# Kernel optimization log

Hardware: AMD Instinct MI355X
Metric: run time of the kernel (lower is better)

## Reference

```python
import jax, jax.numpy as jnp
import numpy as np

B, L, D = 8, 4096, 2048
E, TOPK, RANK = 8, 2, 8
ALPHA = 1.0 / RANK
LN_EPS = 1e-5


def setup_inputs() -> dict:
    key = jax.random.key(0)
    ks = jax.random.split(key, 7)
    return {
        "x": jax.random.normal(ks[0], (B, L, D), dtype=jnp.float32),
        "gate_w": jax.random.normal(ks[1], (E, D), dtype=jnp.float32) * 0.02,
        "gate_b": jax.random.normal(ks[2], (E,), dtype=jnp.float32) * 0.02,
        "A": jax.random.normal(ks[3], (E, RANK, D), dtype=jnp.float32) * 0.02,
        "Bw": jax.random.normal(ks[4], (E, D, RANK), dtype=jnp.float32) * 0.02,
        "gamma": 1.0 + 0.1 * jax.random.normal(ks[5], (D,), dtype=jnp.float32),
        "beta": 0.1 * jax.random.normal(ks[6], (D,), dtype=jnp.float32),
    }


def reference(x, gate_w, gate_b, A, Bw, gamma, beta):
    # pooled hidden state per sequence: [B, D]
    h = x.mean(axis=1)
    # router (eval mode: no jitter noise)
    logits = h @ gate_w.T + gate_b                 # [B, E]
    vals, idx = jax.lax.top_k(logits, TOPK)        # [B, k]
    w = jax.nn.softmax(vals, axis=-1)              # [B, k]

    # ---- auxiliary losses ----
    counts = jnp.sum(jax.nn.one_hot(idx.reshape(-1), E, dtype=logits.dtype), axis=0)
    f = counts / (logits.shape[0] * TOPK)          # fraction routed to each expert
    P = jax.nn.softmax(logits, axis=-1).mean(axis=0)
    load_balance = E * jnp.sum(f * P)
    z_loss = jnp.mean(jax.nn.logsumexp(logits, axis=-1) ** 2)
    p = f + 1e-8
    p = p / p.sum()
    renyi_loss = jnp.log(jnp.sum(p ** 2))          # -(log(sum p^2)/(1-2))*(-1)
    aux = 0.01 * load_balance + 0.001 * z_loss + 0.01 * renyi_loss

    # ---- sparse LoRA expert dispatch (gather selected experts, tiny rank-8 GEMMs) ----
    A_sel = A[idx]                                 # [B, k, r, D]
    B_sel = Bw[idx]                                # [B, k, D, r]
    t = jnp.einsum('bd,bkrd->bkr', h, A_sel)       # [B, k, r]
    expert_out = jnp.einsum('bkr,bkdr->bkd', t, B_sel)  # [B, k, D]
    delta = jnp.sum(w[..., None] * expert_out, axis=1) * ALPHA  # [B, D]

    # residual add + LayerNorm over feature dim
    y = x + delta[:, None, :]
    mu = y.mean(axis=-1, keepdims=True)
    var = y.var(axis=-1, keepdims=True)
    y = (y - mu) / jnp.sqrt(var + LN_EPS) * gamma + beta
    return y, aux
```

## Files before the change

### kernel.cpp

```cpp
#include <hip/hip_runtime.h>
#include <math.h>

#define NB 8
#define NL 4096
#define ND 2048
#define NE 8
#define KTOP 2
#define NR 8
#define ALPHA 0.125f
#define LN_EPS 1e-5f
#define SPLIT 64

typedef float f32x4 __attribute__((ext_vector_type(4)));

__global__ __launch_bounds__(256) void k1_partial_mean(const float* __restrict__ x,
                                                       float* __restrict__ partial) {
    int bid = blockIdx.x;
    int half = bid & 1;
    int b = (bid >> 1) & (NB - 1);
    int s = bid >> 4;
    const int lchunk = NL / SPLIT;
    int d4 = half * 1024 + threadIdx.x * 4;
    const float* xp = x + ((size_t)(b * NL + s * lchunk)) * ND + d4;
    f32x4 a0 = {0.f, 0.f, 0.f, 0.f}, a1 = a0, a2 = a0, a3 = a0;
    f32x4 a4 = a0, a5 = a0, a6 = a0, a7 = a0;
    for (int i = 0; i < lchunk; i += 8) {
        f32x4 v0 = *(const f32x4*)(xp + (size_t)(i + 0) * ND);
        f32x4 v1 = *(const f32x4*)(xp + (size_t)(i + 1) * ND);
        f32x4 v2 = *(const f32x4*)(xp + (size_t)(i + 2) * ND);
        f32x4 v3 = *(const f32x4*)(xp + (size_t)(i + 3) * ND);
        f32x4 v4 = *(const f32x4*)(xp + (size_t)(i + 4) * ND);
        f32x4 v5 = *(const f32x4*)(xp + (size_t)(i + 5) * ND);
        f32x4 v6 = *(const f32x4*)(xp + (size_t)(i + 6) * ND);
        f32x4 v7 = *(const f32x4*)(xp + (size_t)(i + 7) * ND);
        a0 += v0; a1 += v1; a2 += v2; a3 += v3;
        a4 += v4; a5 += v5; a6 += v6; a7 += v7;
    }
    f32x4 acc = ((a0 + a1) + (a2 + a3)) + ((a4 + a5) + (a6 + a7));
    *(f32x4*)(partial + ((size_t)(b * SPLIT + s)) * ND + d4) = acc;
}

__global__ __launch_bounds__(256) void kB_router(const float* __restrict__ partial,
                                                 const float* __restrict__ gate_w,
                                                 const float* __restrict__ gate_b,
                                                 const float* __restrict__ A,
                                                 const float* __restrict__ Bw,
                                                 float* __restrict__ delta,
                                                 float* __restrict__ logits_out,
                                                 int* __restrict__ idx_out) {
    __shared__ float sh_h[ND];
    __shared__ float sh_logits[NE];
    __shared__ float sh_t[KTOP * NR];
    __shared__ float sh_w[KTOP];
    __shared__ int sh_idx[KTOP];
    int b = blockIdx.x;
    int tid = threadIdx.x;

    const float* pb = partial + (size_t)b * SPLIT * ND;
    for (int d4 = tid; d4 < ND / 4; d4 += 256) {
        f32x4 s0 = {0.f, 0.f, 0.f, 0.f}, s1 = s0, s2 = s0, s3 = s0;
#pragma unroll 4
        for (int s = 0; s < SPLIT; s += 4) {
            s0 += *(const f32x4*)(pb + (size_t)(s + 0) * ND + d4 * 4);
            s1 += *(const f32x4*)(pb + (size_t)(s + 1) * ND + d4 * 4);
            s2 += *(const f32x4*)(pb + (size_t)(s + 2) * ND + d4 * 4);
            s3 += *(const f32x4*)(pb + (size_t)(s + 3) * ND + d4 * 4);
        }
        f32x4 r = ((s0 + s1) + (s2 + s3)) * (1.0f / NL);
        *(f32x4*)(sh_h + d4 * 4) = r;
    }
    __syncthreads();

    {
        int e = tid >> 5, lane32 = tid & 31;
        const f32x4* gw = (const f32x4*)(gate_w + (size_t)e * ND);
        float p = 0.f;
#pragma unroll 4
        for (int d4 = lane32; d4 < ND / 4; d4 += 32) {
            f32x4 gv = gw[d4];
            f32x4 hv = *(const f32x4*)(sh_h + d4 * 4);
            p += gv.x * hv.x + gv.y * hv.y + gv.z * hv.z + gv.w * hv.w;
        }
        for (int off = 16; off; off >>= 1) p += __shfl_down(p, off);
        if (lane32 == 0) sh_logits[e] = p + gate_b[e];
    }
    __syncthreads();

    if (tid == 0) {
        float v1 = -1e30f; int e1 = 0;
        for (int e = 0; e < NE; ++e) if (sh_logits[e] > v1) { v1 = sh_logits[e]; e1 = e; }
        float v2 = -1e30f; int e2 = 0;
        for (int e = 0; e < NE; ++e) if (e != e1 && sh_logits[e] > v2) { v2 = sh_logits[e]; e2 = e; }
        float ex = expf(v2 - v1);
        float w1 = 1.0f / (1.0f + ex);
        sh_idx[0] = e1; sh_idx[1] = e2;
        sh_w[0] = w1; sh_w[1] = ex * w1;
        idx_out[b * KTOP] = e1; idx_out[b * KTOP + 1] = e2;
        for (int e = 0; e < NE; ++e) logits_out[b * NE + e] = sh_logits[e];
    }
    __syncthreads();

    {
        int grp = tid >> 4, lane16 = tid & 15;
        int k = grp >> 3, r = grp & 7;
        int e = sh_idx[k];
        const f32x4* ap = (const f32x4*)(A + ((size_t)e * NR + r) * ND);
        float p = 0.f;
#pragma unroll 4
        for (int d4 = lane16; d4 < ND / 4; d4 += 16) {
            f32x4 av = ap[d4];
            f32x4 hv = *(const f32x4*)(sh_h + d4 * 4);
            p += av.x * hv.x + av.y * hv.y + av.z * hv.z + av.w * hv.w;
        }
        for (int off = 8; off; off >>= 1) p += __shfl_down(p, off);
        if (lane16 == 0) sh_t[grp] = p;
    }
    __syncthreads();

    for (int dd = tid; dd < ND; dd += 256) {
        float acc = 0.f;
#pragma unroll
        for (int k = 0; k < KTOP; ++k) {
            int e = sh_idx[k];
            const f32x4* bw = (const f32x4*)(Bw + ((size_t)e * ND + dd) * NR);
            f32x4 w0 = bw[0], w1 = bw[1];
            float s = sh_t[k * NR + 0] * w0.x + sh_t[k * NR + 1] * w0.y +
                      sh_t[k * NR + 2] * w0.z + sh_t[k * NR + 3] * w0.w +
                      sh_t[k * NR + 4] * w1.x + sh_t[k * NR + 5] * w1.y +
                      sh_t[k * NR + 6] * w1.z + sh_t[k * NR + 7] * w1.w;
            acc += sh_w[k] * s;
        }
        delta[b * ND + dd] = acc * ALPHA;
    }
}

__global__ void k3_aux(const float* __restrict__ logits, const int* __restrict__ idxp,
                       float* __restrict__ aux_out) {
    if (threadIdx.x != 0 || blockIdx.x != 0) return;
    float counts[NE];
    for (int e = 0; e < NE; ++e) counts[e] = 0.f;
    for (int i = 0; i < NB * KTOP; ++i) counts[idxp[i]] += 1.f;
    float f[NE], P[NE];
    for (int e = 0; e < NE; ++e) { f[e] = counts[e] * (1.0f / (NB * KTOP)); P[e] = 0.f; }
    float z = 0.f;
    for (int b = 0; b < NB; ++b) {
        const float* lg = logits + b * NE;
        float m = lg[0];
        for (int e = 1; e < NE; ++e) m = fmaxf(m, lg[e]);
        float s = 0.f;
        for (int e = 0; e < NE; ++e) s += expf(lg[e] - m);
        float inv = 1.0f / s;
        for (int e = 0; e < NE; ++e) P[e] += expf(lg[e] - m) * inv;
        float lse = m + logf(s);
        z += lse * lse;
    }
    z *= (1.0f / NB);
    float lb = 0.f;
    for (int e = 0; e < NE; ++e) lb += f[e] * (P[e] * (1.0f / NB));
    lb *= (float)NE;
    float psum = 0.f;
    for (int e = 0; e < NE; ++e) psum += f[e] + 1e-8f;
    float s2 = 0.f;
    for (int e = 0; e < NE; ++e) { float p = (f[e] + 1e-8f) / psum; s2 += p * p; }
    float renyi = logf(s2);
    aux_out[0] = 0.01f * lb + 0.001f * z + 0.01f * renyi;
}

__global__ __launch_bounds__(256) void k4_ln(const float* __restrict__ x,
                                             const float* __restrict__ delta,
                                             const float* __restrict__ gamma,
                                             const float* __restrict__ beta,
                                             float* __restrict__ y) {
    int wave = blockIdx.x * 4 + (threadIdx.x >> 6);
    int lane = threadIdx.x & 63;
    size_t ra = (size_t)wave * ND;
    size_t rb = ((size_t)wave + 16384) * ND;
    int ba = wave >> 12;
    int bb = ba + 4;

    const f32x4* xa = (const f32x4*)(x + ra);
    const f32x4* xb = (const f32x4*)(x + rb);
    const f32x4* da = (const f32x4*)(delta + (size_t)ba * ND);
    const f32x4* db = (const f32x4*)(delta + (size_t)bb * ND);

    f32x4 va[8], vb[8];
#pragma unroll
    for (int j = 0; j < 8; ++j) va[j] = xa[lane + 64 * j];
#pragma unroll
    for (int j = 0; j < 8; ++j) vb[j] = xb[lane + 64 * j];
#pragma unroll
    for (int j = 0; j < 8; ++j) va[j] += da[lane + 64 * j];
#pragma unroll
    for (int j = 0; j < 8; ++j) vb[j] += db[lane + 64 * j];

    float sa = 0.f, ssa = 0.f, sb = 0.f, ssb = 0.f;
#pragma unroll
    for (int j = 0; j < 8; ++j) {
        sa  += va[j].x + va[j].y + va[j].z + va[j].w;
        ssa += va[j].x * va[j].x + va[j].y * va[j].y + va[j].z * va[j].z + va[j].w * va[j].w;
        sb  += vb[j].x + vb[j].y + vb[j].z + vb[j].w;
        ssb += vb[j].x * vb[j].x + vb[j].y * vb[j].y + vb[j].z * vb[j].z + vb[j].w * vb[j].w;
    }
    for (int off = 32; off; off >>= 1) {
        sa  += __shfl_xor(sa, off);
        ssa += __shfl_xor(ssa, off);
        sb  += __shfl_xor(sb, off);
        ssb += __shfl_xor(ssb, off);
    }
    float mua = sa * (1.0f / ND);
    float rsa = rsqrtf(ssa * (1.0f / ND) - mua * mua + LN_EPS);
    float mub = sb * (1.0f / ND);
    float rsb = rsqrtf(ssb * (1.0f / ND) - mub * mub + LN_EPS);

    f32x4* ya = (f32x4*)(y + ra);
    f32x4* yb = (f32x4*)(y + rb);
#pragma unroll
    for (int j = 0; j < 8; ++j) {
        f32x4 gv = *(const f32x4*)(gamma + (lane + 64 * j) * 4);
        f32x4 bv = *(const f32x4*)(beta  + (lane + 64 * j) * 4);
        f32x4 oa = (va[j] - mua) * rsa * gv + bv;
        f32x4 ob = (vb[j] - mub) * rsb * gv + bv;
        __builtin_nontemporal_store(oa, ya + lane + 64 * j);
        __builtin_nontemporal_store(ob, yb + lane + 64 * j);
    }
}

extern "C" void kernel_launch(void* const* d_in, const int* in_sizes, int n_in,
                              void* d_out, int out_size, void* d_ws, size_t ws_size,
                              hipStream_t stream) {
    const float* x      = (const float*)d_in[0];
    const float* gate_w = (const float*)d_in[1];
    const float* gate_b = (const float*)d_in[2];
    const float* A      = (const float*)d_in[3];
    const float* Bw     = (const float*)d_in[4];
    const float* gamma  = (const float*)d_in[5];
    const float* beta   = (const float*)d_in[6];
    float* y   = (float*)d_out;
    float* aux = y + (size_t)NB * NL * ND;

    float* partial = (float*)d_ws;
    float* delta   = partial + (size_t)NB * SPLIT * ND;
    float* logits  = delta + NB * ND;
    int*   idxp    = (int*)(logits + NB * NE);

    hipLaunchKernelGGL(k1_partial_mean, dim3(SPLIT * NB * 2), dim3(256), 0, stream,
                       x, partial);
    hipLaunchKernelGGL(kB_router, dim3(NB), dim3(256), 0, stream,
                       partial, gate_w, gate_b, A, Bw, delta, logits, idxp);
    hipLaunchKernelGGL(k3_aux, dim3(1), dim3(64), 0, stream, logits, idxp, aux);
    hipLaunchKernelGGL(k4_ln, dim3(4096), dim3(256), 0, stream,
                       x, delta, gamma, beta, y);
}
```

Before: 152.8 us.

## Fold aux-loss kernel into LayerNorm kernel and use regular stores

Removes the separate single-thread aux-loss kernel and computes the aux loss in thread 0 of block 0 of the LayerNorm kernel, saving one kernel launch and its dependency gap. It also replaces the nontemporal stores of the output with ordinary stores, which changes how the large output write interacts with the cache. The serial aux computation now sits at the tail of one LN block, which may slightly lengthen that block.

Result: slower. 189.8 us (+24.2%).

```diff
diff --git a/kernel.cpp b/kernel.cpp
--- a/kernel.cpp
+++ b/kernel.cpp
@@ -134,43 +134,14 @@
     }
 }
 
-__global__ void k3_aux(const float* __restrict__ logits, const int* __restrict__ idxp,
-                       float* __restrict__ aux_out) {
-    if (threadIdx.x != 0 || blockIdx.x != 0) return;
-    float counts[NE];
-    for (int e = 0; e < NE; ++e) counts[e] = 0.f;
-    for (int i = 0; i < NB * KTOP; ++i) counts[idxp[i]] += 1.f;
-    float f[NE], P[NE];
-    for (int e = 0; e < NE; ++e) { f[e] = counts[e] * (1.0f / (NB * KTOP)); P[e] = 0.f; }
-    float z = 0.f;
-    for (int b = 0; b < NB; ++b) {
-        const float* lg = logits + b * NE;
-        float m = lg[0];
-        for (int e = 1; e < NE; ++e) m = fmaxf(m, lg[e]);
-        float s = 0.f;
-        for (int e = 0; e < NE; ++e) s += expf(lg[e] - m);
-        float inv = 1.0f / s;
-        for (int e = 0; e < NE; ++e) P[e] += expf(lg[e] - m) * inv;
-        float lse = m + logf(s);
-        z += lse * lse;
-    }
-    z *= (1.0f / NB);
-    float lb = 0.f;
-    for (int e = 0; e < NE; ++e) lb += f[e] * (P[e] * (1.0f / NB));
-    lb *= (float)NE;
-    float psum = 0.f;
-    for (int e = 0; e < NE; ++e) psum += f[e] + 1e-8f;
-    float s2 = 0.f;
-    for (int e = 0; e < NE; ++e) { float p = (f[e] + 1e-8f) / psum; s2 += p * p; }
-    float renyi = logf(s2);
-    aux_out[0] = 0.01f * lb + 0.001f * z + 0.01f * renyi;
-}
-
 __global__ __launch_bounds__(256) void k4_ln(const float* __restrict__ x,
                                              const float* __restrict__ delta,
                                              const float* __restrict__ gamma,
                                              const float* __restrict__ beta,
-                                             float* __restrict__ y) {
+                                             const float* __restrict__ logits,
+                                             const int* __restrict__ idxp,
+                                             float* __restrict__ y,
+                                             float* __restrict__ aux_out) {
     int wave = blockIdx.x * 4 + (threadIdx.x >> 6);
     int lane = threadIdx.x & 63;
     size_t ra = (size_t)wave * ND;
@@ -218,10 +189,37 @@
     for (int j = 0; j < 8; ++j) {
         f32x4 gv = *(const f32x4*)(gamma + (lane + 64 * j) * 4);
         f32x4 bv = *(const f32x4*)(beta  + (lane + 64 * j) * 4);
-        f32x4 oa = (va[j] - mua) * rsa * gv + bv;
-        f32x4 ob = (vb[j] - mub) * rsb * gv + bv;
-        __builtin_nontemporal_store(oa, ya + lane + 64 * j);
-        __builtin_nontemporal_store(ob, yb + lane + 64 * j);
+        ya[lane + 64 * j] = (va[j] - mua) * rsa * gv + bv;
+        yb[lane + 64 * j] = (vb[j] - mub) * rsb * gv + bv;
+    }
+
+    if (blockIdx.x == 0 && threadIdx.x == 0) {
+        float counts[NE];
+        for (int e = 0; e < NE; ++e) counts[e] = 0.f;
+        for (int i = 0; i < NB * KTOP; ++i) counts[idxp[i]] += 1.f;
+        float f[NE], P[NE];
+        for (int e = 0; e < NE; ++e) { f[e] = counts[e] * (1.0f / (NB * KTOP)); P[e] = 0.f; }
+        float z = 0.f;
+        for (int bq = 0; bq < NB; ++bq) {
+            const float* lg = logits + bq * NE;
+            float m = lg[0];
+            for (int e = 1; e < NE; ++e) m = fmaxf(m, lg[e]);
+            float sum = 0.f;
+            for (int e = 0; e < NE; ++e) sum += expf(lg[e] - m);
+            float inv = 1.0f / sum;
+            for (int e = 0; e < NE; ++e) P[e] += expf(lg[e] - m) * inv;
+            float lse = m + logf(sum);
+            z += lse * lse;
+        }
+        z *= (1.0f / NB);
+        float lb = 0.f;
+        for (int e = 0; e < NE; ++e) lb += f[e] * (P[e] * (1.0f / NB));
+        lb *= (float)NE;
+        float psum = 0.f;
+        for (int e = 0; e < NE; ++e) psum += f[e] + 1e-8f;
+        float s2 = 0.f;
+        for (int e = 0; e < NE; ++e) { float p = (f[e] + 1e-8f) / psum; s2 += p * p; }
+        aux_out[0] = 0.01f * lb + 0.001f * z + 0.01f * logf(s2);
     }
 }
 
@@ -247,7 +245,6 @@
                        x, partial);
     hipLaunchKernelGGL(kB_router, dim3(NB), dim3(256), 0, stream,
                        partial, gate_w, gate_b, A, Bw, delta, logits, idxp);
-    hipLaunchKernelGGL(k3_aux, dim3(1), dim3(64), 0, stream, logits, idxp, aux);
     hipLaunchKernelGGL(k4_ln, dim3(4096), dim3(256), 0, stream,
-                       x, delta, gamma, beta, y);
-}
+                       x, delta, gamma, beta, logits, idxp, y, aux);
+}
```
